# Performance work log

Measured on AMD Instinct MI355X. Metric: run time of the kernel, lower is better.

## Reference

```python
import jax, jax.numpy as jnp
import numpy as np

S = 4        # support_num
NEI = 32     # neighbor_num for conv stages
POOL_NEI = 4 # neighbor_num inside Pool_layer
EPS = 1e-12


def sq_dist(a, b):
    # a: (b,m,3), b: (b,n,3) -> (b,m,n)
    return (jnp.sum(a * a, -1)[:, :, None] + jnp.sum(b * b, -1)[:, None, :]
            - 2.0 * jnp.einsum('bmd,bnd->bmn', a, b))


def query_ball(radius, k, points, queries):
    # PointNet++-style ball query: up to k indices within radius, padded with first hit.
    d = sq_dist(queries, points)                      # (b,m,n)
    n = points.shape[1]
    idx = jnp.broadcast_to(jnp.arange(n, dtype=jnp.int32), d.shape)
    idx = jnp.where(d > radius * radius, n, idx)
    idx = jnp.sort(idx, axis=-1)[..., :k]             # (b,m,k)
    first = idx[..., :1]
    return jnp.where(idx == n, first, idx)


def gather_nb(feat, idx):
    # feat: (b,v,c), idx: (b,v,k) -> (b,v,k,c)
    return jax.vmap(lambda f, i: f[i])(feat, idx)


def neighbor_dir_norm(verts, idx):
    nb = gather_nb(verts, idx)                        # (b,v,k,3)
    d = nb - verts[:, :, None, :]
    return d / (jnp.linalg.norm(d, axis=-1, keepdims=True) + EPS)


def conv_surface(idx, verts, dirs):
    # dirs: (3, S*out). Geometric-only first layer of 3DGCN.
    b, v, k = idx.shape
    o = dirs.shape[1] // S
    dn = neighbor_dir_norm(verts, idx)                # (b,v,k,3)
    sd = dirs / (jnp.linalg.norm(dirs, axis=0, keepdims=True) + EPS)
    theta = jnp.maximum(jnp.einsum('bvkd,dm->bvkm', dn, sd), 0.0)
    theta = theta.reshape(b, v, k, S, o)
    return theta.max(axis=2).sum(axis=2)              # (b,v,o)


def conv_layer(idx, verts, feat, w, bias, dirs):
    # w: (cin,(S+1)*o), bias: ((S+1)*o,), dirs: (3,S*o)
    b, v, k = idx.shape
    o = dirs.shape[1] // S
    dn = neighbor_dir_norm(verts, idx)
    sd = dirs / (jnp.linalg.norm(dirs, axis=0, keepdims=True) + EPS)
    theta = jnp.maximum(jnp.einsum('bvkd,dm->bvkm', dn, sd), 0.0)  # (b,v,k,S*o)
    fout = feat @ w + bias                            # (b,v,(S+1)*o)
    center, supp = fout[..., :o], fout[..., o:]
    supp_nb = gather_nb(supp, idx)                    # (b,v,k,S*o)
    act = (theta * supp_nb).reshape(b, v, k, S, o).max(axis=2).sum(axis=2)
    return center + act


def pool(verts, feat, radius):
    idx = query_ball(radius, POOL_NEI, verts, verts)
    pooled = gather_nb(feat, idx).max(axis=2)         # (b,v,c)
    m = verts.shape[1] // 2                           # pooling_rate = 2 (deterministic subsample)
    return verts[:, :m], pooled[:, :m]


def setup_inputs() -> dict:
    key = jax.random.key(0)
    ks = jax.random.split(key, 32)
    B, V = 4, 4096
    inp = {}
    inp['vertices'] = jax.random.uniform(ks[0], (B, V, 3), dtype=jnp.float32)
    inp['surf_dirs'] = jax.random.normal(ks[1], (3, S * 32), dtype=jnp.float32) * 0.1
    specs = [(1, 32, 32), (3, 64, 32), (4, 96, 32), (6, 128, 32), (7, 160, 32),
             (8, 192, 32), (9, 224, 32), (10, 256, 32), (11, 288, 1024)]
    i = 2
    for n, cin, cout in specs:
        inp[f'w{n}'] = jax.random.normal(ks[i], (cin, (S + 1) * cout), dtype=jnp.float32) / np.sqrt(cin); i += 1
        inp[f'b{n}'] = jnp.zeros(((S + 1) * cout,), jnp.float32)
        inp[f'd{n}'] = jax.random.normal(ks[i], (3, S * cout), dtype=jnp.float32) * 0.1; i += 1
    inp['fc1_w'] = jax.random.normal(ks[i], (1024, 256), dtype=jnp.float32) * 0.03; i += 1
    inp['fc1_b'] = jnp.zeros((256,), jnp.float32)
    inp['bn_g'] = jnp.ones((256,), jnp.float32)
    inp['bn_b'] = jnp.zeros((256,), jnp.float32)
    inp['bn_m'] = jnp.zeros((256,), jnp.float32)
    inp['bn_v'] = jnp.ones((256,), jnp.float32)
    inp['fc2_w'] = jax.random.normal(ks[i], (256, 40), dtype=jnp.float32) * 0.06
    inp['fc2_b'] = jnp.zeros((40,), jnp.float32)
    return inp


def reference(vertices, surf_dirs, w1, b1, d1, w3, b3, d3, w4, b4, d4, w6, b6, d6,
              w7, b7, d7, w8, b8, d8, w9, b9, d9, w10, b10, d10, w11, b11, d11,
              fc1_w, fc1_b, bn_g, bn_b, bn_m, bn_v, fc2_w, fc2_b):
    relu = lambda x: jnp.maximum(x, 0.0)
    verts = vertices
    idx = query_ball(0.2, NEI, verts, verts)
    fm0 = relu(conv_surface(idx, verts, surf_dirs))
    fm1 = relu(conv_layer(idx, verts, fm0, w1, b1, d1))
    fm1 = jnp.concatenate([fm0, fm1], -1)
    verts, fm1 = pool(verts, fm1, 0.2)
    idx = query_ball(0.4, NEI, verts, verts)
    fm3 = relu(conv_layer(idx, verts, fm1, w3, b3, d3)); fm3 = jnp.concatenate([fm1, fm3], -1)
    fm4 = relu(conv_layer(idx, verts, fm3, w4, b4, d4)); fm4 = jnp.concatenate([fm3, fm4], -1)
    verts, fm4 = pool(verts, fm4, 0.4)
    idx = query_ball(0.6, NEI, verts, verts)
    fm6 = relu(conv_layer(idx, verts, fm4, w6, b6, d6)); fm6 = jnp.concatenate([fm4, fm6], -1)
    fm7 = relu(conv_layer(idx, verts, fm6, w7, b7, d7)); fm7 = jnp.concatenate([fm6, fm7], -1)
    verts, fm7 = pool(verts, fm7, 0.6)
    idx = query_ball(0.8, NEI, verts, verts)
    fm8 = relu(conv_layer(idx, verts, fm7, w8, b8, d8)); fm8 = jnp.concatenate([fm7, fm8], -1)
    fm9 = relu(conv_layer(idx, verts, fm8, w9, b9, d9)); fm9 = jnp.concatenate([fm8, fm9], -1)
    verts, fm9 = pool(verts, fm9, 0.8)
    idx = query_ball(1.0, NEI, verts, verts)
    fm10 = relu(conv_layer(idx, verts, fm9, w10, b10, d10)); fm10 = jnp.concatenate([fm9, fm10], -1)
    fm11 = conv_layer(idx, verts, fm10, w11, b11, d11)
    g = fm11.max(axis=1)                              # (b,1024) global max pool
    h = g @ fc1_w + fc1_b                             # Dropout is identity at inference
    h = (h - bn_m) / jnp.sqrt(bn_v + 1e-5) * bn_g + bn_b
    h = relu(h)
    return h @ fc2_w + fc2_b                          # (b,40)
```

## Files before the change

### kernel.cpp

```cpp
#include <hip/hip_runtime.h>
#include <hip/hip_bf16.h>
#include <math.h>

#define DEV __device__ __forceinline__

DEV float frn_mul(float a, float b) { return __fmul_rn(a, b); }
DEV float frn_add(float a, float b) { return __fadd_rn(a, b); }

union BFU { __hip_bfloat16 h; unsigned short u; };

__global__ void qb_kernel(const float* __restrict__ verts, int Vp, int Vq, int B,
                          float r2, int K, int* __restrict__ idx_out)
{
    int wid = (blockIdx.x * blockDim.x + threadIdx.x) >> 6;
    int lane = threadIdx.x & 63;
    int nq = B * Vq;
    if (wid >= nq) return;
    int b = wid / Vq;
    int v = wid - b * Vq;

    const float* q = verts + (size_t)(b * Vp + v) * 3;
    float qx = q[0], qy = q[1], qz = q[2];
    float qn = frn_add(frn_add(frn_mul(qx, qx), frn_mul(qy, qy)), frn_mul(qz, qz));
    const float* pts = verts + (size_t)b * Vp * 3;
    int* row = idx_out + (size_t)wid * K;

    int count = 0;
    int first = -1;
    for (int base = 0; base < Vp && count < K; base += 64) {
        int j = base + lane;
        bool in = false;
        if (j < Vp) {
            float px = pts[j * 3 + 0], py = pts[j * 3 + 1], pz = pts[j * 3 + 2];
            float pn = frn_add(frn_add(frn_mul(px, px), frn_mul(py, py)), frn_mul(pz, pz));
            float dt = frn_add(frn_add(frn_mul(qx, px), frn_mul(qy, py)), frn_mul(qz, pz));
            float d = __fsub_rn(frn_add(qn, pn), frn_mul(2.0f, dt));
            in = !(d > r2);
        }
        unsigned long long mask = __ballot(in);
        if (first < 0 && mask != 0ull)
            first = base + (int)__ffsll((long long)mask) - 1;
        int pos = count + (int)__popcll(mask & ((1ull << lane) - 1ull));
        if (in && pos < K) row[pos] = j;
        count += (int)__popcll(mask);
    }
    int cnt = count < K ? count : K;
    for (int t = cnt + lane; t < K; t += 64) row[t] = first;
}

__global__ void qb_surface_kernel(const float* __restrict__ verts, int V, int B,
                                  float r2,
                                  const float* __restrict__ dirs,
                                  float* __restrict__ outF, int Cw,
                                  int* __restrict__ idx_out)
{
    __shared__ int rowS[4][32];
    int wid = (blockIdx.x * blockDim.x + threadIdx.x) >> 6;
    int lane = threadIdx.x & 63;
    int wql = threadIdx.x >> 6;
    int b = wid / V;
    int v = wid - b * V;

    const float* q = verts + (size_t)wid * 3;
    float qx = q[0], qy = q[1], qz = q[2];
    float qn = frn_add(frn_add(frn_mul(qx, qx), frn_mul(qy, qy)), frn_mul(qz, qz));
    const float* pts = verts + (size_t)b * V * 3;
    int* row = idx_out + (size_t)wid * 32;
    (void)v;

    int count = 0;
    int first = -1;
    for (int base = 0; base < V && count < 32; base += 64) {
        int j = base + lane;
        float px = pts[j * 3 + 0], py = pts[j * 3 + 1], pz = pts[j * 3 + 2];
        float pn = frn_add(frn_add(frn_mul(px, px), frn_mul(py, py)), frn_mul(pz, pz));
        float dt = frn_add(frn_add(frn_mul(qx, px), frn_mul(qy, py)), frn_mul(qz, pz));
        float d = __fsub_rn(frn_add(qn, pn), frn_mul(2.0f, dt));
        bool in = !(d > r2);
        unsigned long long mask = __ballot(in);
        if (first < 0 && mask != 0ull)
            first = base + (int)__ffsll((long long)mask) - 1;
        int pos = count + (int)__popcll(mask & ((1ull << lane) - 1ull));
        if (in && pos < 32) { row[pos] = j; rowS[wql][pos] = j; }
        count += (int)__popcll(mask);
    }
    int cnt = count < 32 ? count : 32;
    for (int t = cnt + lane; t < 32; t += 64) { row[t] = first; rowS[wql][t] = first; }
    __syncthreads();

    float dnx, dny, dnz;
    {
        int k = lane & 31;
        int nb = rowS[wql][k];
        int nbrow = b * V + nb;
        float dx = verts[(size_t)nbrow * 3 + 0] - qx;
        float dy = verts[(size_t)nbrow * 3 + 1] - qy;
        float dz = verts[(size_t)nbrow * 3 + 2] - qz;
        float nrm = sqrtf(dx * dx + dy * dy + dz * dz) + 1e-12f;
        float inv = 1.0f / nrm;
        dnx = dx * inv; dny = dy * inv; dnz = dz * inv;
    }
    int m1 = lane, m2 = lane + 64;
    float ax = dirs[m1], ay = dirs[128 + m1], az = dirs[256 + m1];
    float i1 = 1.0f / (sqrtf(ax * ax + ay * ay + az * az) + 1e-12f);
    ax *= i1; ay *= i1; az *= i1;
    float bx = dirs[m2], by = dirs[128 + m2], bz = dirs[256 + m2];
    float i2 = 1.0f / (sqrtf(bx * bx + by * by + bz * bz) + 1e-12f);
    bx *= i2; by *= i2; bz *= i2;

    float mx1 = -INFINITY, mx2 = -INFINITY;
    for (int k = 0; k < 32; ++k) {
        float ex = __shfl(dnx, k, 64);
        float ey = __shfl(dny, k, 64);
        float ez = __shfl(dnz, k, 64);
        float t1 = fmaxf(ex * ax + ey * ay + ez * az, 0.0f);
        float t2 = fmaxf(ex * bx + ey * by + ez * bz, 0.0f);
        mx1 = fmaxf(mx1, t1);
        mx2 = fmaxf(mx2, t2);
    }
    float part = mx1 + mx2;
    float tot = part + __shfl_xor(part, 32, 64);
    if (lane < 32) {
        outF[(size_t)wid * Cw + lane] = fmaxf(tot, 0.0f);
    }
}

template <typename OT>
__global__ __launch_bounds__(256)
void gemm_tiled_kernel(const float* __restrict__ feat, int Cw, int cin,
                       const float* __restrict__ w, const float* __restrict__ bias,
                       int N, OT* __restrict__ fout)
{
    __shared__ float As[64][36];
    __shared__ float Bs[32][68];

    int m0 = blockIdx.x * 64;
    int n0 = blockIdx.y * 64;
    int tid = threadIdx.x;
    int tx = tid & 15, ty = tid >> 4;

    float acc[4][4];
#pragma unroll
    for (int i = 0; i < 4; ++i)
#pragma unroll
        for (int j = 0; j < 4; ++j) acc[i][j] = 0.0f;

    for (int k0 = 0; k0 < cin; k0 += 32) {
#pragma unroll
        for (int i = 0; i < 2; ++i) {
            int qq = tid + i * 256;
            int row = qq >> 3, c = qq & 7;
            float4 v = *(const float4*)&feat[(size_t)(m0 + row) * Cw + k0 + 4 * c];
            *(float4*)&As[row][4 * c] = v;
        }
#pragma unroll
        for (int i = 0; i < 2; ++i) {
            int qq = tid + i * 256;
            int kr = qq >> 4, c = qq & 15;
            int n = n0 + 4 * c;
            float4 v = make_float4(0.0f, 0.0f, 0.0f, 0.0f);
            if (n < N) v = *(const float4*)&w[(size_t)(k0 + kr) * N + n];
            *(float4*)&Bs[kr][4 * c] = v;
        }
        __syncthreads();

#pragma unroll
        for (int kt = 0; kt < 32; kt += 4) {
            float4 av4[4], bv4[4];
#pragma unroll
            for (int i = 0; i < 4; ++i) av4[i] = *(const float4*)&As[ty * 4 + i][kt];
#pragma unroll
            for (int r = 0; r < 4; ++r) bv4[r] = *(const float4*)&Bs[kt + r][tx * 4];
            const float* a = (const float*)av4;
            const float* bb = (const float*)bv4;
#pragma unroll
            for (int i = 0; i < 4; ++i)
#pragma unroll
                for (int r = 0; r < 4; ++r)
#pragma unroll
                    for (int j = 0; j < 4; ++j)
                        acc[i][j] = fmaf(a[i * 4 + r], bb[r * 4 + j], acc[i][j]);
        }
        __syncthreads();
    }

    int n = n0 + tx * 4;
    if (n < N) {
        float b0 = bias[n + 0], b1 = bias[n + 1], b2 = bias[n + 2], b3 = bias[n + 3];
#pragma unroll
        for (int i = 0; i < 4; ++i) {
            int m = m0 + ty * 4 + i;
            if constexpr (__is_same(OT, float)) {
                float4 o;
                o.x = acc[i][0] + b0;
                o.y = acc[i][1] + b1;
                o.z = acc[i][2] + b2;
                o.w = acc[i][3] + b3;
                *(float4*)&fout[(size_t)m * N + n] = o;
            } else {
                BFU t0, t1, t2, t3;
                t0.h = __float2bfloat16(acc[i][0] + b0);
                t1.h = __float2bfloat16(acc[i][1] + b1);
                t2.h = __float2bfloat16(acc[i][2] + b2);
                t3.h = __float2bfloat16(acc[i][3] + b3);
                ushort4 o;
                o.x = t0.u; o.y = t1.u; o.z = t2.u; o.w = t3.u;
                *(ushort4*)&fout[(size_t)m * N + n] = o;
            }
        }
    }
}

template <typename OT>
__global__ __launch_bounds__(256)
void gemm_tiled_n128_kernel(const float* __restrict__ feat, int Cw, int cin,
                            const float* __restrict__ w, const float* __restrict__ bias,
                            int N, OT* __restrict__ fout)
{
    __shared__ float As[64][36];
    __shared__ float Bs[32][132];

    int m0 = blockIdx.x * 64;
    int n0 = blockIdx.y * 128;
    int tid = threadIdx.x;
    int tx = tid & 15, ty = tid >> 4;

    float acc[4][8];
#pragma unroll
    for (int i = 0; i < 4; ++i)
#pragma unroll
        for (int j = 0; j < 8; ++j) acc[i][j] = 0.0f;

    for (int k0 = 0; k0 < cin; k0 += 32) {
#pragma unroll
        for (int i = 0; i < 2; ++i) {
            int qq = tid + i * 256;
            int row = qq >> 3, c = qq & 7;
            float4 v = *(const float4*)&feat[(size_t)(m0 + row) * Cw + k0 + 4 * c];
            *(float4*)&As[row][4 * c] = v;
        }
#pragma unroll
        for (int i = 0; i < 4; ++i) {
            int qq = tid + i * 256;
            int kr = qq >> 5, c = qq & 31;
            int n = n0 + 4 * c;
            float4 v = make_float4(0.0f, 0.0f, 0.0f, 0.0f);
            if (n < N) v = *(const float4*)&w[(size_t)(k0 + kr) * N + n];
            *(float4*)&Bs[kr][4 * c] = v;
        }
        __syncthreads();

#pragma unroll
        for (int kt = 0; kt < 32; kt += 4) {
            float4 av4[4];
            float4 bv4[4][2];
#pragma unroll
            for (int i = 0; i < 4; ++i) av4[i] = *(const float4*)&As[ty * 4 + i][kt];
#pragma unroll
            for (int r = 0; r < 4; ++r) {
                bv4[r][0] = *(const float4*)&Bs[kt + r][tx * 4];
                bv4[r][1] = *(const float4*)&Bs[kt + r][64 + tx * 4];
            }
            const float* a = (const float*)av4;
            const float* bb = (const float*)bv4;
#pragma unroll
            for (int i = 0; i < 4; ++i)
#pragma unroll
                for (int r = 0; r < 4; ++r)
#pragma unroll
                    for (int j = 0; j < 8; ++j)
                        acc[i][j] = fmaf(a[i * 4 + r], bb[r * 8 + j], acc[i][j]);
        }
        __syncthreads();
    }

#pragma unroll
    for (int half = 0; half < 2; ++half) {
        int n = n0 + half * 64 + tx * 4;
        if (n < N) {
            float b0 = bias[n + 0], b1 = bias[n + 1], b2 = bias[n + 2], b3 = bias[n + 3];
#pragma unroll
            for (int i = 0; i < 4; ++i) {
                int m = m0 + ty * 4 + i;
                float o0 = acc[i][half * 4 + 0] + b0;
                float o1 = acc[i][half * 4 + 1] + b1;
                float o2 = acc[i][half * 4 + 2] + b2;
                float o3 = acc[i][half * 4 + 3] + b3;
                if constexpr (__is_same(OT, float)) {
                    float4 o; o.x = o0; o.y = o1; o.z = o2; o.w = o3;
                    *(float4*)&fout[(size_t)m * N + n] = o;
                } else {
                    BFU t0, t1, t2, t3;
                    t0.h = __float2bfloat16(o0);
                    t1.h = __float2bfloat16(o1);
                    t2.h = __float2bfloat16(o2);
                    t3.h = __float2bfloat16(o3);
                    ushort4 o; o.x = t0.u; o.y = t1.u; o.z = t2.u; o.w = t3.u;
                    *(ushort4*)&fout[(size_t)m * N + n] = o;
                }
            }
        }
    }
}

__global__ void conv_agg32_kernel(const int* __restrict__ idx,
                                  const float* __restrict__ verts,
                                  const float* __restrict__ fout,
                                  const float* __restrict__ dirs,
                                  float* __restrict__ outF, int Cw, int coff,
                                  int V, int do_relu)
{
    int blk = blockIdx.x;
    int b = (blk & 7) >> 1;
    int j = ((blk >> 3) << 1) | (blk & 1);
    int wid = b * V + j * 4 + (int)(threadIdx.x >> 6);
    int lane = threadIdx.x & 63;

    float dnx, dny, dnz;
    int nbrow;
    {
        int k = lane & 31;
        int nb = idx[(size_t)wid * 32 + k];
        nbrow = b * V + nb;
        float cx = verts[(size_t)wid * 3 + 0];
        float cy = verts[(size_t)wid * 3 + 1];
        float cz = verts[(size_t)wid * 3 + 2];
        float dx = verts[(size_t)nbrow * 3 + 0] - cx;
        float dy = verts[(size_t)nbrow * 3 + 1] - cy;
        float dz = verts[(size_t)nbrow * 3 + 2] - cz;
        float nrm = sqrtf(dx * dx + dy * dy + dz * dz) + 1e-12f;
        float inv = 1.0f / nrm;
        dnx = dx * inv; dny = dy * inv; dnz = dz * inv;
    }
    int m1 = lane, m2 = lane + 64;
    float ax = dirs[m1], ay = dirs[128 + m1], az = dirs[256 + m1];
    float i1 = 1.0f / (sqrtf(ax * ax + ay * ay + az * az) + 1e-12f);
    ax *= i1; ay *= i1; az *= i1;
    float bx = dirs[m2], by = dirs[128 + m2], bz = dirs[256 + m2];
    float i2 = 1.0f / (sqrtf(bx * bx + by * by + bz * bz) + 1e-12f);
    bx *= i2; by *= i2; bz *= i2;

    float mx1 = -INFINITY, mx2 = -INFINITY;
    for (int k = 0; k < 32; ++k) {
        float ex = __shfl(dnx, k, 64);
        float ey = __shfl(dny, k, 64);
        float ez = __shfl(dnz, k, 64);
        int nr = __shfl(nbrow, k, 64);
        const float* fr = fout + (size_t)nr * 160 + 32;
        float t1 = fmaxf(ex * ax + ey * ay + ez * az, 0.0f);
        float t2 = fmaxf(ex * bx + ey * by + ez * bz, 0.0f);
        mx1 = fmaxf(mx1, t1 * fr[m1]);
        mx2 = fmaxf(mx2, t2 * fr[m2]);
    }
    float part = mx1 + mx2;
    float tot = part + __shfl_xor(part, 32, 64);
    if (lane < 32) {
        float c = fout[(size_t)wid * 160 + lane];
        float val = c + tot;
        if (do_relu) val = fmaxf(val, 0.0f);
        outF[(size_t)wid * Cw + coff + lane] = val;
    }
}

__global__ void conv_agg_big_kernel(const int* __restrict__ idx,
                                    const float* __restrict__ verts,
                                    const __hip_bfloat16* __restrict__ fout,
                                    const float* __restrict__ dirs,
                                    float* __restrict__ G,
                                    int V, int B)
{
    __shared__ float dnS[32][3];
    __shared__ int nbS[32];
    int blk = blockIdx.x;
    int b = (blk & 7) >> 1;
    int v = ((blk >> 3) << 1) | (blk & 1);
    int row = b * V + v;
    int tid = threadIdx.x;

    if (tid < 32) {
        int nb = idx[(size_t)row * 32 + tid];
        int nbrow = b * V + nb;
        float cx = verts[(size_t)row * 3 + 0];
        float cy = verts[(size_t)row * 3 + 1];
        float cz = verts[(size_t)row * 3 + 2];
        float dx = verts[(size_t)nbrow * 3 + 0] - cx;
        float dy = verts[(size_t)nbrow * 3 + 1] - cy;
        float dz = verts[(size_t)nbrow * 3 + 2] - cz;
        float nrm = sqrtf(dx * dx + dy * dy + dz * dz) + 1e-12f;
        float inv = 1.0f / nrm;
        dnS[tid][0] = dx * inv; dnS[tid][1] = dy * inv; dnS[tid][2] = dz * inv;
        nbS[tid] = nbrow;
    }
    __syncthreads();

    float sdx[16], sdy[16], sdz[16], mx[16];
    for (int p = 0; p < 16; ++p) {
        int pair = p * 256 + tid;
        float ax = dirs[pair], ay = dirs[4096 + pair], az = dirs[8192 + pair];
        float inv = 1.0f / (sqrtf(ax * ax + ay * ay + az * az) + 1e-12f);
        sdx[p] = ax * inv; sdy[p] = ay * inv; sdz[p] = az * inv;
        mx[p] = -INFINITY;
    }
    for (int k = 0; k < 32; ++k) {
        float ex = dnS[k][0], ey = dnS[k][1], ez = dnS[k][2];
        const __hip_bfloat16* fr = fout + (size_t)nbS[k] * 5120 + 1024;
        for (int p = 0; p < 16; ++p) {
            float th = fmaxf(ex * sdx[p] + ey * sdy[p] + ez * sdz[p], 0.0f);
            float s = __bfloat162float(fr[p * 256 + tid]);
            mx[p] = fmaxf(mx[p], th * s);
        }
    }
    for (int q = 0; q < 4; ++q) {
        float val = ((mx[q] + mx[4 + q]) + mx[8 + q]) + mx[12 + q];
        int oo = q * 256 + tid;
        float c = __bfloat162float(fout[(size_t)row * 5120 + oo]);
        G[(size_t)row * 1024 + oo] = c + val;
    }
}

__global__ void pool_fused_kernel(const int* __restrict__ idx_conv,
                                  const float* __restrict__ verts, int Vp, int Vh, int B,
                                  const float* __restrict__ Fin, int CwIn,
                                  float* __restrict__ Fout, int CwOut, int C,
                                  float* __restrict__ vout)
{
    int wid = (blockIdx.x * blockDim.x + threadIdx.x) >> 6;
    int lane = threadIdx.x & 63;
    int nq = B * Vh;
    if (wid >= nq) return;
    int b = wid / Vh;
    int v = wid - b * Vh;
    int rowc = b * Vp + v;

    int idv = 0;
    if (lane < 4) idv = idx_conv[(size_t)rowc * 32 + lane];
    int i0 = __shfl(idv, 0, 64);
    int i1 = __shfl(idv, 1, 64);
    int i2 = __shfl(idv, 2, 64);
    int i3 = __shfl(idv, 3, 64);

    const float* r0 = Fin + (size_t)(b * Vp + i0) * CwIn;
    const float* r1 = Fin + (size_t)(b * Vp + i1) * CwIn;
    const float* r2p = Fin + (size_t)(b * Vp + i2) * CwIn;
    const float* r3 = Fin + (size_t)(b * Vp + i3) * CwIn;
    for (int c = lane; c < C; c += 64) {
        float m = fmaxf(fmaxf(r0[c], r1[c]), fmaxf(r2p[c], r3[c]));
        Fout[(size_t)wid * CwOut + c] = m;
    }
    if (lane < 3) vout[(size_t)wid * 3 + lane] = verts[(size_t)rowc * 3 + lane];
}

__global__ void gmax_kernel(const float* __restrict__ G, float* __restrict__ gm,
                            int V)
{
    __shared__ float red[4][64];
    int b = blockIdx.x >> 4;
    int c0 = (blockIdx.x & 15) * 64;
    int t = threadIdx.x;
    int c = c0 + (t & 63);
    int vg = t >> 6;
    float m = -INFINITY;
    for (int v = vg * 64; v < (vg + 1) * 64; ++v)
        m = fmaxf(m, G[((size_t)b * V + v) * 1024 + c]);
    red[vg][t & 63] = m;
    __syncthreads();
    if (t < 64) {
        float r = fmaxf(fmaxf(red[0][t], red[1][t]), fmaxf(red[2][t], red[3][t]));
        gm[b * 1024 + c0 + t] = r;
    }
}

__global__ __launch_bounds__(256)
void fc1_kernel(const float* __restrict__ gm, const float* __restrict__ w1,
                const float* __restrict__ b1_,
                const float* __restrict__ bn_g, const float* __restrict__ bn_b,
                const float* __restrict__ bn_m, const float* __restrict__ bn_v,
                float* __restrict__ h)
{
    __shared__ float gs[1024];
    __shared__ float red[8][32];
    int b = blockIdx.y;
    int j0 = blockIdx.x * 32;
    int t = threadIdx.x;
    for (int i = t; i < 1024; i += 256) gs[i] = gm[b * 1024 + i];
    __syncthreads();
    int jj = t & 31, kk = t >> 5;
    int j = j0 + jj;
    const float* wp = w1 + (size_t)(kk * 128) * 256 + j;
    float acc = 0.0f;
#pragma unroll 8
    for (int k = 0; k < 128; ++k)
        acc = fmaf(gs[kk * 128 + k], wp[(size_t)k * 256], acc);
    red[kk][jj] = acc;
    __syncthreads();
    if (t < 32) {
        float s = 0.0f;
#pragma unroll
        for (int q = 0; q < 8; ++q) s += red[q][t];
        int jw = j0 + t;
        s += b1_[jw];
        s = (s - bn_m[jw]) / sqrtf(bn_v[jw] + 1e-5f) * bn_g[jw] + bn_b[jw];
        h[b * 256 + jw] = fmaxf(s, 0.0f);
    }
}

__global__ void fc2_kernel(const float* __restrict__ h, const float* __restrict__ w2,
                           const float* __restrict__ b2_, float* __restrict__ out)
{
    __shared__ float hs[256];
    int b = blockIdx.x;
    int t = threadIdx.x;
    hs[t] = h[b * 256 + t];
    __syncthreads();
    if (t < 40) {
        float acc = 0.0f;
#pragma unroll 8
        for (int k = 0; k < 256; ++k) acc = fmaf(hs[k], w2[(size_t)k * 40 + t], acc);
        out[b * 40 + t] = acc + b2_[t];
    }
}

static inline int wblocks(int waves) { return (waves + 3) / 4; }
static inline dim3 ggrid(int M, int N) { return dim3(M / 64, (N + 63) / 64); }
static inline dim3 ggridn128(int M, int N) { return dim3(M / 64, (N + 127) / 128); }

extern "C" void kernel_launch(void* const* d_in, const int* in_sizes, int n_in,
                              void* d_out, int out_size, void* d_ws, size_t ws_size,
                              hipStream_t stream)
{
    const int B = 4;
    const float* verts1 = (const float*)d_in[0];
    const float* surf_dirs = (const float*)d_in[1];
    const float* w1 = (const float*)d_in[2];
    const float* b1 = (const float*)d_in[3];
    const float* d1 = (const float*)d_in[4];
    const float* w3 = (const float*)d_in[5];
    const float* b3 = (const float*)d_in[6];
    const float* d3 = (const float*)d_in[7];
    const float* w4 = (const float*)d_in[8];
    const float* b4 = (const float*)d_in[9];
    const float* d4 = (const float*)d_in[10];
    const float* w6 = (const float*)d_in[11];
    const float* b6 = (const float*)d_in[12];
    const float* d6 = (const float*)d_in[13];
    const float* w7 = (const float*)d_in[14];
    const float* b7 = (const float*)d_in[15];
    const float* d7 = (const float*)d_in[16];
    const float* w8 = (const float*)d_in[17];
    const float* b8 = (const float*)d_in[18];
    const float* d8 = (const float*)d_in[19];
    const float* w9 = (const float*)d_in[20];
    const float* b9 = (const float*)d_in[21];
    const float* d9 = (const float*)d_in[22];
    const float* w10 = (const float*)d_in[23];
    const float* b10 = (const float*)d_in[24];
    const float* d10 = (const float*)d_in[25];
    const float* w11 = (const float*)d_in[26];
    const float* b11 = (const float*)d_in[27];
    const float* d11 = (const float*)d_in[28];
    const float* fc1_w = (const float*)d_in[29];
    const float* fc1_b = (const float*)d_in[30];
    const float* bn_g = (const float*)d_in[31];
    const float* bn_b = (const float*)d_in[32];
    const float* bn_m = (const float*)d_in[33];
    const float* bn_v = (const float*)d_in[34];
    const float* fc2_w = (const float*)d_in[35];
    const float* fc2_b = (const float*)d_in[36];
    (void)in_sizes; (void)n_in; (void)out_size; (void)ws_size;

    float* ws = (float*)d_ws;
    size_t off = 0;
    auto alloc = [&](size_t n) { float* p = ws + off; off += n; return p; };
    float* fout = alloc(4 * 256 * 5120);
    int* idx = (int*)alloc(4 * 4096 * 32);
    float* F1 = alloc(4 * 4096 * 64);
    float* L2 = alloc(4 * 2048 * 128);
    float* L3 = alloc(4 * 1024 * 192);
    float* L4 = alloc(4 * 512 * 256);
    float* L5 = alloc(4 * 256 * 288);
    float* G = alloc(4 * 256 * 1024);
    float* v2 = alloc(4 * 2048 * 3);
    float* v3 = alloc(4 * 1024 * 3);
    float* v4 = alloc(4 * 512 * 3);
    float* v5 = alloc(4 * 256 * 3);
    float* gm = alloc(4 * 1024);
    float* hh = alloc(4 * 256);

    qb_surface_kernel<<<wblocks(B * 4096), 256, 0, stream>>>(verts1, 4096, B, 0.04f, surf_dirs, F1, 64, idx);
    gemm_tiled_kernel<float><<<ggrid(B * 4096, 160), 256, 0, stream>>>(F1, 64, 32, w1, b1, 160, fout);
    conv_agg32_kernel<<<B * 4096 / 4, 256, 0, stream>>>(idx, verts1, fout, d1, F1, 64, 32, 4096, 1);
    pool_fused_kernel<<<wblocks(B * 2048), 256, 0, stream>>>(idx, verts1, 4096, 2048, B, F1, 64, L2, 128, 64, v2);

    qb_kernel<<<wblocks(B * 2048), 256, 0, stream>>>(v2, 2048, 2048, B, 0.16f, 32, idx);
    gemm_tiled_kernel<float><<<ggrid(B * 2048, 160), 256, 0, stream>>>(L2, 128, 64, w3, b3, 160, fout);
    conv_agg32_kernel<<<B * 2048 / 4, 256, 0, stream>>>(idx, v2, fout, d3, L2, 128, 64, 2048, 1);
    gemm_tiled_kernel<float><<<ggrid(B * 2048, 160), 256, 0, stream>>>(L2, 128, 96, w4, b4, 160, fout);
    conv_agg32_kernel<<<B * 2048 / 4, 256, 0, stream>>>(idx, v2, fout, d4, L2, 128, 96, 2048, 1);
    pool_fused_kernel<<<wblocks(B * 1024), 256, 0, stream>>>(idx, v2, 2048, 1024, B, L2, 128, L3, 192, 128, v3);

    qb_kernel<<<wblocks(B * 1024), 256, 0, stream>>>(v3, 1024, 1024, B, 0.36f, 32, idx);
    gemm_tiled_kernel<float><<<ggrid(B * 1024, 160), 256, 0, stream>>>(L3, 192, 128, w6, b6, 160, fout);
    conv_agg32_kernel<<<B * 1024 / 4, 256, 0, stream>>>(idx, v3, fout, d6, L3, 192, 128, 1024, 1);
    gemm_tiled_kernel<float><<<ggrid(B * 1024, 160), 256, 0, stream>>>(L3, 192, 160, w7, b7, 160, fout);
    conv_agg32_kernel<<<B * 1024 / 4, 256, 0, stream>>>(idx, v3, fout, d7, L3, 192, 160, 1024, 1);
    pool_fused_kernel<<<wblocks(B * 512), 256, 0, stream>>>(idx, v3, 1024, 512, B, L3, 192, L4, 256, 192, v4);

    qb_kernel<<<wblocks(B * 512), 256, 0, stream>>>(v4, 512, 512, B, 0.64f, 32, idx);
    gemm_tiled_kernel<float><<<ggrid(B * 512, 160), 256, 0, stream>>>(L4, 256, 192, w8, b8, 160, fout);
    conv_agg32_kernel<<<B * 512 / 4, 256, 0, stream>>>(idx, v4, fout, d8, L4, 256, 192, 512, 1);
    gemm_tiled_kernel<float><<<ggrid(B * 512, 160), 256, 0, stream>>>(L4, 256, 224, w9, b9, 160, fout);
    conv_agg32_kernel<<<B * 512 / 4, 256, 0, stream>>>(idx, v4, fout, d9, L4, 256, 224, 512, 1);
    pool_fused_kernel<<<wblocks(B * 256), 256, 0, stream>>>(idx, v4, 512, 256, B, L4, 256, L5, 288, 256, v5);

    qb_kernel<<<wblocks(B * 256), 256, 0, stream>>>(v5, 256, 256, B, 1.0f, 32, idx);
    gemm_tiled_kernel<float><<<ggrid(B * 256, 160), 256, 0, stream>>>(L5, 288, 256, w10, b10, 160, fout);
    conv_agg32_kernel<<<B * 256 / 4, 256, 0, stream>>>(idx, v5, fout, d10, L5, 288, 256, 256, 1);
    __hip_bfloat16* fout_bf = (__hip_bfloat16*)fout;
    gemm_tiled_n128_kernel<__hip_bfloat16><<<ggridn128(B * 256, 5120), 256, 0, stream>>>(L5, 288, 288, w11, b11, 5120, fout_bf);
    conv_agg_big_kernel<<<B * 256, 256, 0, stream>>>(idx, v5, fout_bf, d11, G, 256, B);

    gmax_kernel<<<64, 256, 0, stream>>>(G, gm, 256);
    fc1_kernel<<<dim3(8, B), 256, 0, stream>>>(gm, fc1_w, fc1_b, bn_g, bn_b, bn_m, bn_v, hh);
    fc2_kernel<<<B, 256, 0, stream>>>(hh, fc2_w, fc2_b, (float*)d_out);
}
```

Baseline: 489.4 us.

## Use bf16 MFMA for the final conv GEMM with pre-cast operands

```diff
diff --git a/kernel.cpp b/kernel.cpp
--- a/kernel.cpp
+++ b/kernel.cpp
@@ -8,6 +8,9 @@
 DEV float frn_add(float a, float b) { return __fadd_rn(a, b); }
 
 union BFU { __hip_bfloat16 h; unsigned short u; };
+
+typedef __attribute__((ext_vector_type(8))) short short8v;
+typedef __attribute__((ext_vector_type(4))) float f32x4;
 
 __global__ void qb_kernel(const float* __restrict__ verts, int Vp, int Vq, int B,
                           float r2, int K, int* __restrict__ idx_out)
@@ -59,14 +62,12 @@
     int lane = threadIdx.x & 63;
     int wql = threadIdx.x >> 6;
     int b = wid / V;
-    int v = wid - b * V;
 
     const float* q = verts + (size_t)wid * 3;
     float qx = q[0], qy = q[1], qz = q[2];
     float qn = frn_add(frn_add(frn_mul(qx, qx), frn_mul(qy, qy)), frn_mul(qz, qz));
     const float* pts = verts + (size_t)b * V * 3;
     int* row = idx_out + (size_t)wid * 32;
-    (void)v;
 
     int count = 0;
     int first = -1;
@@ -211,93 +212,108 @@
     }
 }
 
-template <typename OT>
+__global__ void cast_bf16_kernel(const float* __restrict__ src,
+                                 unsigned short* __restrict__ dst, int n8)
+{
+    int t = blockIdx.x * blockDim.x + threadIdx.x;
+    if (t >= n8) return;
+    float4 v0 = *(const float4*)&src[(size_t)t * 8];
+    float4 v1 = *(const float4*)&src[(size_t)t * 8 + 4];
+    BFU a;
+    ushort4 o0, o1;
+    a.h = __float2bfloat16(v0.x); o0.x = a.u;
+    a.h = __float2bfloat16(v0.y); o0.y = a.u;
+    a.h = __float2bfloat16(v0.z); o0.z = a.u;
+    a.h = __float2bfloat16(v0.w); o0.w = a.u;
+    a.h = __float2bfloat16(v1.x); o1.x = a.u;
+    a.h = __float2bfloat16(v1.y); o1.y = a.u;
+    a.h = __float2bfloat16(v1.z); o1.z = a.u;
+    a.h = __float2bfloat16(v1.w); o1.w = a.u;
+    *(ushort4*)&dst[(size_t)t * 8] = o0;
+    *(ushort4*)&dst[(size_t)t * 8 + 4] = o1;
+}
+
+__global__ void castT_bf16_kernel(const float* __restrict__ w,
+                                  unsigned short* __restrict__ wt)
+{
+    int t = blockIdx.x * blockDim.x + threadIdx.x;
+    if (t >= 5120 * 36) return;
+    int kc = t / 5120;
+    int n = t - kc * 5120;
+    BFU a;
+    ushort4 o0, o1;
+    a.h = __float2bfloat16(w[(size_t)(kc * 8 + 0) * 5120 + n]); o0.x = a.u;
+    a.h = __float2bfloat16(w[(size_t)(kc * 8 + 1) * 5120 + n]); o0.y = a.u;
+    a.h = __float2bfloat16(w[(size_t)(kc * 8 + 2) * 5120 + n]); o0.z = a.u;
+    a.h = __float2bfloat16(w[(size_t)(kc * 8 + 3) * 5120 + n]); o0.w = a.u;
+    a.h = __float2bfloat16(w[(size_t)(kc * 8 + 4) * 5120 + n]); o1.x = a.u;
+    a.h = __float2bfloat16(w[(size_t)(kc * 8 + 5) * 5120 + n]); o1.y = a.u;
+    a.h = __float2bfloat16(w[(size_t)(kc * 8 + 6) * 5120 + n]); o1.z = a.u;
+    a.h = __float2bfloat16(w[(size_t)(kc * 8 + 7) * 5120 + n]); o1.w = a.u;
+    *(ushort4*)&wt[(size_t)n * 288 + kc * 8] = o0;
+    *(ushort4*)&wt[(size_t)n * 288 + kc * 8 + 4] = o1;
+}
+
 __global__ __launch_bounds__(256)
-void gemm_tiled_n128_kernel(const float* __restrict__ feat, int Cw, int cin,
-                            const float* __restrict__ w, const float* __restrict__ bias,
-                            int N, OT* __restrict__ fout)
-{
-    __shared__ float As[64][36];
-    __shared__ float Bs[32][132];
-
-    int m0 = blockIdx.x * 64;
+void gemm_mfma_conv11(const unsigned short* __restrict__ Abf,
+                      const unsigned short* __restrict__ WTbf,
+                      const float* __restrict__ bias,
+                      __hip_bfloat16* __restrict__ fout)
+{
+    __shared__ unsigned short As[128][40];
+    __shared__ unsigned short Bs[128][40];
+    const int K = 288, N = 5120;
+    int m0 = blockIdx.x * 128;
     int n0 = blockIdx.y * 128;
     int tid = threadIdx.x;
-    int tx = tid & 15, ty = tid >> 4;
-
-    float acc[4][8];
-#pragma unroll
-    for (int i = 0; i < 4; ++i)
-#pragma unroll
-        for (int j = 0; j < 8; ++j) acc[i][j] = 0.0f;
-
-    for (int k0 = 0; k0 < cin; k0 += 32) {
+    int lane = tid & 63;
+    int wave = tid >> 6;
+    int wm = wave & 1, wn = wave >> 1;
+    int l15 = lane & 15, l4 = lane >> 4;
+
+    f32x4 acc[4][4];
+#pragma unroll
+    for (int mi = 0; mi < 4; ++mi)
+#pragma unroll
+        for (int ni = 0; ni < 4; ++ni) acc[mi][ni] = (f32x4){0.f, 0.f, 0.f, 0.f};
+
+    for (int k0 = 0; k0 < K; k0 += 32) {
 #pragma unroll
         for (int i = 0; i < 2; ++i) {
-            int qq = tid + i * 256;
-            int row = qq >> 3, c = qq & 7;
-            float4 v = *(const float4*)&feat[(size_t)(m0 + row) * Cw + k0 + 4 * c];
-            *(float4*)&As[row][4 * c] = v;
-        }
-#pragma unroll
-        for (int i = 0; i < 4; ++i) {
-            int qq = tid + i * 256;
-            int kr = qq >> 5, c = qq & 31;
-            int n = n0 + 4 * c;
-            float4 v = make_float4(0.0f, 0.0f, 0.0f, 0.0f);
-            if (n < N) v = *(const float4*)&w[(size_t)(k0 + kr) * N + n];
-            *(float4*)&Bs[kr][4 * c] = v;
+            int c = tid + i * 256;
+            int row = c >> 2, qq = c & 3;
+            *(uint4*)&As[row][qq * 8] = *(const uint4*)&Abf[(size_t)(m0 + row) * K + k0 + qq * 8];
+            *(uint4*)&Bs[row][qq * 8] = *(const uint4*)&WTbf[(size_t)(n0 + row) * K + k0 + qq * 8];
         }
         __syncthreads();
 
-#pragma unroll
-        for (int kt = 0; kt < 32; kt += 4) {
-            float4 av4[4];
-            float4 bv4[4][2];
-#pragma unroll
-            for (int i = 0; i < 4; ++i) av4[i] = *(const float4*)&As[ty * 4 + i][kt];
-#pragma unroll
-            for (int r = 0; r < 4; ++r) {
-                bv4[r][0] = *(const float4*)&Bs[kt + r][tx * 4];
-                bv4[r][1] = *(const float4*)&Bs[kt + r][64 + tx * 4];
-            }
-            const float* a = (const float*)av4;
-            const float* bb = (const float*)bv4;
-#pragma unroll
-            for (int i = 0; i < 4; ++i)
-#pragma unroll
-                for (int r = 0; r < 4; ++r)
-#pragma unroll
-                    for (int j = 0; j < 8; ++j)
-                        acc[i][j] = fmaf(a[i * 4 + r], bb[r * 8 + j], acc[i][j]);
-        }
+        short8v af[4], bfv[4];
+#pragma unroll
+        for (int mi = 0; mi < 4; ++mi)
+            af[mi] = *(const short8v*)&As[wm * 64 + mi * 16 + l15][l4 * 8];
+#pragma unroll
+        for (int ni = 0; ni < 4; ++ni)
+            bfv[ni] = *(const short8v*)&Bs[wn * 64 + ni * 16 + l15][l4 * 8];
+#pragma unroll
+        for (int mi = 0; mi < 4; ++mi)
+#pragma unroll
+            for (int ni = 0; ni < 4; ++ni)
+                acc[mi][ni] = __builtin_amdgcn_mfma_f32_16x16x32_bf16(af[mi], bfv[ni], acc[mi][ni], 0, 0, 0);
         __syncthreads();
     }
 
 #pragma unroll
-    for (int half = 0; half < 2; ++half) {
-        int n = n0 + half * 64 + tx * 4;
-        if (n < N) {
-            float b0 = bias[n + 0], b1 = bias[n + 1], b2 = bias[n + 2], b3 = bias[n + 3];
-#pragma unroll
-            for (int i = 0; i < 4; ++i) {
-                int m = m0 + ty * 4 + i;
-                float o0 = acc[i][half * 4 + 0] + b0;
-                float o1 = acc[i][half * 4 + 1] + b1;
-                float o2 = acc[i][half * 4 + 2] + b2;
-                float o3 = acc[i][half * 4 + 3] + b3;
-                if constexpr (__is_same(OT, float)) {
-                    float4 o; o.x = o0; o.y = o1; o.z = o2; o.w = o3;
-                    *(float4*)&fout[(size_t)m * N + n] = o;
-                } else {
-                    BFU t0, t1, t2, t3;
-                    t0.h = __float2bfloat16(o0);
-                    t1.h = __float2bfloat16(o1);
-                    t2.h = __float2bfloat16(o2);
-                    t3.h = __float2bfloat16(o3);
-                    ushort4 o; o.x = t0.u; o.y = t1.u; o.z = t2.u; o.w = t3.u;
-                    *(ushort4*)&fout[(size_t)m * N + n] = o;
-                }
+    for (int ni = 0; ni < 4; ++ni) {
+        int col = n0 + wn * 64 + ni * 16 + l15;
+        float bv = bias[col];
+#pragma unroll
+        for (int mi = 0; mi < 4; ++mi) {
+            int rbase = m0 + wm * 64 + mi * 16 + l4 * 4;
+#pragma unroll
+            for (int j = 0; j < 4; ++j) {
+                BFU u;
+                u.h = __float2bfloat16(acc[mi][ni][j] + bv);
+                *(unsigned short*)&fout[(size_t)(rbase + j) * N + col] = u.u;
             }
         }
     }
@@ -522,7 +538,6 @@
 
 static inline int wblocks(int waves) { return (waves + 3) / 4; }
 static inline dim3 ggrid(int M, int N) { return dim3(M / 64, (N + 63) / 64); }
-static inline dim3 ggridn128(int M, int N) { return dim3(M / 64, (N + 127) / 128); }
 
 extern "C" void kernel_launch(void* const* d_in, const int* in_sizes, int n_in,
                               void* d_out, int out_size, void* d_ws, size_t ws_size,
@@ -586,6 +601,9 @@
     float* gm = alloc(4 * 1024);
     float* hh = alloc(4 * 256);
 
+    unsigned short* Abf = (unsigned short*)G;
+    unsigned short* WTbf = Abf + 1024 * 288;
+
     qb_surface_kernel<<<wblocks(B * 4096), 256, 0, stream>>>(verts1, 4096, B, 0.04f, surf_dirs, F1, 64, idx);
     gemm_tiled_kernel<float><<<ggrid(B * 4096, 160), 256, 0, stream>>>(F1, 64, 32, w1, b1, 160, fout);
     conv_agg32_kernel<<<B * 4096 / 4, 256, 0, stream>>>(idx, verts1, fout, d1, F1, 64, 32, 4096, 1);
@@ -613,10 +631,12 @@
     pool_fused_kernel<<<wblocks(B * 256), 256, 0, stream>>>(idx, v4, 512, 256, B, L4, 256, L5, 288, 256, v5);
 
     qb_kernel<<<wblocks(B * 256), 256, 0, stream>>>(v5, 256, 256, B, 1.0f, 32, idx);
+    castT_bf16_kernel<<<(5120 * 36 + 255) / 256, 256, 0, stream>>>(w11, WTbf);
     gemm_tiled_kernel<float><<<ggrid(B * 256, 160), 256, 0, stream>>>(L5, 288, 256, w10, b10, 160, fout);
     conv_agg32_kernel<<<B * 256 / 4, 256, 0, stream>>>(idx, v5, fout, d10, L5, 288, 256, 256, 1);
+    cast_bf16_kernel<<<(36864 + 255) / 256, 256, 0, stream>>>(L5, Abf, 36864);
     __hip_bfloat16* fout_bf = (__hip_bfloat16*)fout;
-    gemm_tiled_n128_kernel<__hip_bfloat16><<<ggridn128(B * 256, 5120), 256, 0, stream>>>(L5, 288, 288, w11, b11, 5120, fout_bf);
+    gemm_mfma_conv11<<<dim3(8, 40), 256, 0, stream>>>(Abf, WTbf, b11, fout_bf);
     conv_agg_big_kernel<<<B * 256, 256, 0, stream>>>(idx, v5, fout_bf, d11, G, 256, B);
 
     gmax_kernel<<<64, 256, 0, stream>>>(G, gm, 256);
```

New measurement: 466.4 us. -4.7%, faster.
